# Performance work log

Measured on AMD Instinct MI355X. Metric: run time of the kernel, lower is better.

## Reference

```python
import jax, jax.numpy as jnp
import numpy as np

L, D, H, FF = 4, 256, 8, 4 * 256  # num_layers, d_model, nhead, ffn hidden
DK = D // H
EPS = 1e-5


def _ln(x, g, b):
    mu = jnp.mean(x, axis=-1, keepdims=True)
    var = jnp.mean(jnp.square(x - mu), axis=-1, keepdims=True)
    return (x - mu) * jax.lax.rsqrt(var + EPS) * g + b


def setup_inputs() -> dict:
    key = jax.random.key(0)
    ks = jax.random.split(key, 16)
    B, N = 8, 1024
    s = 0.02
    return {
        "x": jax.random.normal(ks[0], (B, N, D), jnp.float32),
        "coords": jax.random.normal(ks[1], (B, N, 3), jnp.float32),
        "Wq": jax.random.normal(ks[2], (L, D, D), jnp.float32) * s,
        "bq": jnp.zeros((L, D), jnp.float32),
        "Wk": jax.random.normal(ks[3], (L, D, D), jnp.float32) * s,
        "bk": jnp.zeros((L, D), jnp.float32),
        "Wv": jax.random.normal(ks[4], (L, D, D), jnp.float32) * s,
        "bv": jnp.zeros((L, D), jnp.float32),
        "alpha": jnp.full((L,), 0.1, jnp.float32),
        "W1": jax.random.normal(ks[5], (L, D, FF), jnp.float32) * s,
        "b1": jnp.zeros((L, FF), jnp.float32),
        "W2": jax.random.normal(ks[6], (L, FF, D), jnp.float32) * s,
        "b2": jnp.zeros((L, D), jnp.float32),
        "g1": jnp.ones((L, D), jnp.float32),
        "be1": jnp.zeros((L, D), jnp.float32),
        "g2": jnp.ones((L, D), jnp.float32),
        "be2": jnp.zeros((L, D), jnp.float32),
    }


def reference(x, coords, Wq, bq, Wk, bk, Wv, bv, alpha, W1, b1, W2, b2, g1, be1, g2, be2):
    B, N, _ = x.shape
    # Per-batch pairwise coord dot products (same math as the BN x BN matmul
    # sliced per batch in the original, computed without the cross-batch waste).
    G0 = jnp.einsum("bnc,bmc->bnm", coords, coords)  # [B,N,N]
    scale = 1.0 / jnp.sqrt(jnp.float32(DK))
    for i in range(L):
        q = (x @ Wq[i] + bq[i]).reshape(B, N, H, DK)
        k = (x @ Wk[i] + bk[i]).reshape(B, N, H, DK)
        v = (x @ Wv[i] + bv[i]).reshape(B, N, H, DK)
        scores = jnp.einsum("bnhd,bmhd->bhnm", q, k) * scale + (alpha[i] * G0)[:, None]
        attn = jax.nn.softmax(scores, axis=-1)
        out = jnp.einsum("bhnm,bmhd->bnhd", attn, v).reshape(B, N, D)
        x = _ln(x + out, g1[i], be1[i])
        ff = jnp.maximum(x @ W1[i] + b1[i], 0.0) @ W2[i] + b2[i]
        x = _ln(x + ff, g2[i], be2[i])
    return x
```

## Files before the change

kernel.cpp:

```cpp
#include <hip/hip_runtime.h>
#include <hip/hip_bf16.h>

#define BB 8
#define NN 1024
#define DD 256
#define HH 8
#define DK 32
#define FFN 1024
#define NLAYERS 4
#define MM (BB * NN)
#define ROW_ELEMS (MM * DD)

#define QSCALE 0.2550655192922103f
#define LOG2E  1.4426950408889634f

typedef unsigned short ushort_t;
typedef __attribute__((ext_vector_type(8))) short bf16x8;
typedef __attribute__((ext_vector_type(4))) short bf16x4;
typedef __attribute__((ext_vector_type(4))) float f32x4;

__device__ __forceinline__ f32x4 mfma16(bf16x4 a, bf16x4 b, f32x4 c) {
#if __has_builtin(__builtin_amdgcn_mfma_f32_16x16x16bf16_1k)
    return __builtin_amdgcn_mfma_f32_16x16x16bf16_1k(a, b, c, 0, 0, 0);
#elif defined(__AMDGCN__)
    f32x4 d;
    asm volatile("v_mfma_f32_16x16x16_bf16 %0, %1, %2, %3"
                 : "=v"(d)
                 : "v"(a), "v"(b), "v"(c));
    return d;
#else
    return c;
#endif
}

__device__ __forceinline__ ushort_t f2b(float f) {
    __hip_bfloat16 h = __float2bfloat16(f);
    return *reinterpret_cast<ushort_t*>(&h);
}

__device__ __forceinline__ float fast_exp2(float x) {
#if __has_builtin(__builtin_amdgcn_exp2f)
    return __builtin_amdgcn_exp2f(x);
#else
    return exp2f(x);
#endif
}

__device__ __forceinline__ void async_ld16(const void* g, void* l) {
    __builtin_amdgcn_global_load_lds((const __attribute__((address_space(1))) void*)g,
                                     (__attribute__((address_space(3))) void*)l, 16, 0, 0);
}

__global__ __launch_bounds__(256) void copy_in_kernel(const float* __restrict__ in,
                                                      float* __restrict__ xf,
                                                      ushort_t* __restrict__ xb, int n) {
    int i = blockIdx.x * 256 + threadIdx.x;
    if (i < n) { float v = in[i]; xf[i] = v; xb[i] = f2b(v); }
}

__global__ __launch_bounds__(256) void prep_kernel(const float* __restrict__ Wq,
                                                   const float* __restrict__ Wk,
                                                   const float* __restrict__ Wv,
                                                   const float* __restrict__ W1,
                                                   const float* __restrict__ W2,
                                                   const float* __restrict__ bq,
                                                   const float* __restrict__ bk,
                                                   const float* __restrict__ bv,
                                                   ushort_t* __restrict__ wqkvt,
                                                   ushort_t* __restrict__ w1t,
                                                   ushort_t* __restrict__ w2t,
                                                   float* __restrict__ bqkv) {
    const int id = blockIdx.x;
    const int layer = id / 707;
    const int r = id % 707;
    const int tid = threadIdx.x;

    if (r >= 704) {
        const int chunk = r - 704;
        const float* src = (chunk == 0) ? bq : (chunk == 1) ? bk : bv;
        bqkv[layer * 768 + chunk * 256 + tid] = src[layer * 256 + tid];
        return;
    }

    const float* src;
    ushort_t* dst;
    int R, C, x, y;
    if (r < 192) {
        const int w = r >> 6, rr = r & 63;
        src = ((w == 0) ? Wq : (w == 1) ? Wk : Wv) + (size_t)layer * 65536;
        dst = wqkvt + (size_t)layer * 196608 + w * 65536;
        R = 256; C = 256; x = rr & 7; y = rr >> 3;
    } else if (r < 448) {
        const int rr = r - 192;
        src = W1 + (size_t)layer * 262144;
        dst = w1t + (size_t)layer * 262144;
        R = 256; C = 1024; x = rr & 31; y = rr >> 5;
    } else {
        const int rr = r - 448;
        src = W2 + (size_t)layer * 262144;
        dst = w2t + (size_t)layer * 262144;
        R = 1024; C = 256; x = rr & 7; y = rr >> 3;
    }
    const int r0 = y * 32, c0 = x * 32;
    __shared__ float tile[32][33];
    const int tx = tid & 31, ty = tid >> 5;
#pragma unroll
    for (int i = 0; i < 4; ++i)
        tile[ty + 8 * i][tx] = src[(size_t)(r0 + ty + 8 * i) * C + (c0 + tx)];
    __syncthreads();
#pragma unroll
    for (int i = 0; i < 4; ++i)
        dst[(size_t)(c0 + ty + 8 * i) * R + (r0 + tx)] = f2b(tile[tx][ty + 8 * i]);
}

template <int MODE, int BM>
__global__ __launch_bounds__(256) void mfma_gemm_kernel(const ushort_t* __restrict__ A,
                                                        const ushort_t* __restrict__ Bt,
                                                        const float* __restrict__ bias,
                                                        void* __restrict__ C0,
                                                        void* __restrict__ C1,
                                                        void* __restrict__ C2,
                                                        const float* __restrict__ coords,
                                                        const float* __restrict__ alpha, int layer,
                                                        int K, int ldc) {
    constexpr int NI = BM / 32;
    __shared__ ushort_t As0[BM * 32];
    __shared__ ushort_t As1[BM * 32];
    __shared__ ushort_t Bs0[128 * 32];
    __shared__ ushort_t Bs1[128 * 32];

    const int t    = threadIdx.x;
    const int bm   = blockIdx.y * BM;
    const int bn   = blockIdx.x * 128;
    const int wave = t >> 6, lane = t & 63;
    const int wm   = (wave >> 1) * (BM / 2), wn = (wave & 1) * 64;
    const int quad = lane >> 4, l16 = lane & 15;

    const int srow = t >> 2;
    const int scol = (t & 3) * 8;

    f32x4 acc[NI][4];
#pragma unroll
    for (int i = 0; i < NI; ++i)
#pragma unroll
        for (int j = 0; j < 4; ++j) {
            f32x4 z = {0.f, 0.f, 0.f, 0.f};
            acc[i][j] = z;
        }

    for (int k0 = 0; k0 < K; k0 += 64) {
        __syncthreads();
        async_ld16(A + (size_t)(bm + srow) * K + k0 + scol, As0 + wave * 512);
        if constexpr (BM == 128)
            async_ld16(A + (size_t)(bm + 64 + srow) * K + k0 + scol, As0 + 2048 + wave * 512);
        async_ld16(Bt + (size_t)(bn + srow) * K + k0 + scol, Bs0 + wave * 512);
        async_ld16(Bt + (size_t)(bn + 64 + srow) * K + k0 + scol, Bs0 + 2048 + wave * 512);
        async_ld16(A + (size_t)(bm + srow) * K + k0 + 32 + scol, As1 + wave * 512);
        if constexpr (BM == 128)
            async_ld16(A + (size_t)(bm + 64 + srow) * K + k0 + 32 + scol, As1 + 2048 + wave * 512);
        async_ld16(Bt + (size_t)(bn + srow) * K + k0 + 32 + scol, Bs1 + wave * 512);
        async_ld16(Bt + (size_t)(bn + 64 + srow) * K + k0 + 32 + scol, Bs1 + 2048 + wave * 512);
        __syncthreads();

        bf16x8 af0[NI], af1[NI], bf0[4], bf1[4];
#pragma unroll
        for (int i = 0; i < NI; ++i) {
            af0[i] = *(const bf16x8*)(As0 + (wm + i * 16 + l16) * 32 + quad * 8);
            af1[i] = *(const bf16x8*)(As1 + (wm + i * 16 + l16) * 32 + quad * 8);
        }
#pragma unroll
        for (int j = 0; j < 4; ++j) {
            bf0[j] = *(const bf16x8*)(Bs0 + (wn + j * 16 + l16) * 32 + quad * 8);
            bf1[j] = *(const bf16x8*)(Bs1 + (wn + j * 16 + l16) * 32 + quad * 8);
        }
#pragma unroll
        for (int i = 0; i < NI; ++i)
#pragma unroll
            for (int j = 0; j < 4; ++j) {
                acc[i][j] = __builtin_amdgcn_mfma_f32_16x16x32_bf16(af0[i], bf0[j], acc[i][j], 0, 0, 0);
                acc[i][j] = __builtin_amdgcn_mfma_f32_16x16x32_bf16(af1[i], bf1[j], acc[i][j], 0, 0, 0);
            }
    }

    const float av = (MODE == 2) ? alpha[layer] : 0.f;

#pragma unroll
    for (int j = 0; j < 4; ++j) {
        const int col = bn + wn + j * 16 + l16;
        const float bsv = bias[col];
#pragma unroll
        for (int i = 0; i < NI; ++i) {
            const int row0 = bm + wm + i * 16 + quad * 4;
            if (MODE == 2) {
                const int bb2 = row0 >> 10, nn0 = row0 & 1023;
                const int which = col >> 8, rem = col & 255;
                const int h = rem >> 5, d = rem & 31;
                const size_t bh = (size_t)((bb2 << 3) + h);
                if (which == 2) {
                    ushort4 pk;
                    pk.x = f2b(acc[i][j][0] + bsv);
                    pk.y = f2b(acc[i][j][1] + bsv);
                    pk.z = f2b(acc[i][j][2] + bsv);
                    pk.w = f2b(acc[i][j][3] + bsv);
                    *(ushort4*)&((ushort_t*)C2)[(bh * DK + d) * NN + nn0] = pk;
                } else {
#pragma unroll
                    for (int r = 0; r < 4; ++r) {
                        const float v = acc[i][j][r] + bsv;
                        const int nn = nn0 + r;
                        if (which == 0) {
                            ((ushort_t*)C0)[(bh * NN + nn) * 64 + d] = f2b(v * QSCALE);
                            ushort_t ext = 0;
                            if (d < 3) ext = f2b(av * LOG2E * coords[(size_t)(bb2 * NN + nn) * 3 + d]);
                            ((ushort_t*)C0)[(bh * NN + nn) * 64 + 32 + d] = ext;
                        } else {
                            ((ushort_t*)C1)[(bh * NN + nn) * 64 + d] = f2b(v);
                            ushort_t ext = 0;
                            if (d < 3) ext = f2b(coords[(size_t)(bb2 * NN + nn) * 3 + d]);
                            ((ushort_t*)C1)[(bh * NN + nn) * 64 + 32 + d] = ext;
                        }
                    }
                }
            } else {
#pragma unroll
                for (int r = 0; r < 4; ++r) {
                    float v = acc[i][j][r] + bsv;
                    if (MODE == 0)
                        ((float*)C0)[(size_t)(row0 + r) * ldc + col] = v;
                    else
                        ((ushort_t*)C0)[(size_t)(row0 + r) * ldc + col] = f2b(fmaxf(v, 0.f));
                }
            }
        }
    }
}

__global__ __launch_bounds__(512) void ff2ln_kernel(const ushort_t* __restrict__ A,
                                                    const ushort_t* __restrict__ Bt,
                                                    const float* __restrict__ bias,
                                                    const float* __restrict__ xres,
                                                    const float* __restrict__ g,
                                                    const float* __restrict__ be,
                                                    float* __restrict__ xout,
                                                    ushort_t* __restrict__ xb) {
    constexpr int K = FFN;
    __shared__ ushort_t As0[32 * 32];
    __shared__ ushort_t As1[32 * 32];
    __shared__ ushort_t Bs0[256 * 32];
    __shared__ ushort_t Bs1[256 * 32];
    __shared__ float redS[8][32];
    __shared__ float redQ[8][32];

    const int t = threadIdx.x;
    const int bm = blockIdx.x * 32;
    const int wave = t >> 6, lane = t & 63;
    const int quad = lane >> 4, l16 = lane & 15;
    const int wn = wave * 32;
    const int srow = t >> 2;
    const int scol = (t & 3) * 8;

    f32x4 acc[2][2];
#pragma unroll
    for (int i = 0; i < 2; ++i)
#pragma unroll
        for (int j = 0; j < 2; ++j) {
            f32x4 z = {0.f, 0.f, 0.f, 0.f};
            acc[i][j] = z;
        }

    for (int k0 = 0; k0 < K; k0 += 64) {
        __syncthreads();
        if (t < 128) {
            async_ld16(A + (size_t)(bm + srow) * K + k0 + scol, As0 + wave * 512);
        } else if (t < 256) {
            async_ld16(A + (size_t)(bm + srow - 32) * K + k0 + 32 + scol, As1 + (wave - 2) * 512);
        }
        async_ld16(Bt + (size_t)srow * K + k0 + scol, Bs0 + wave * 512);
        async_ld16(Bt + (size_t)(128 + srow) * K + k0 + scol, Bs0 + 4096 + wave * 512);
        async_ld16(Bt + (size_t)srow * K + k0 + 32 + scol, Bs1 + wave * 512);
        async_ld16(Bt + (size_t)(128 + srow) * K + k0 + 32 + scol, Bs1 + 4096 + wave * 512);
        __syncthreads();

        bf16x8 af0[2], af1[2], bf0[2], bf1[2];
#pragma unroll
        for (int i = 0; i < 2; ++i) {
            af0[i] = *(const bf16x8*)(As0 + (i * 16 + l16) * 32 + quad * 8);
            af1[i] = *(const bf16x8*)(As1 + (i * 16 + l16) * 32 + quad * 8);
        }
#pragma unroll
        for (int j = 0; j < 2; ++j) {
            bf0[j] = *(const bf16x8*)(Bs0 + (wn + j * 16 + l16) * 32 + quad * 8);
            bf1[j] = *(const bf16x8*)(Bs1 + (wn + j * 16 + l16) * 32 + quad * 8);
        }
#pragma unroll
        for (int i = 0; i < 2; ++i)
#pragma unroll
            for (int j = 0; j < 2; ++j) {
                acc[i][j] = __builtin_amdgcn_mfma_f32_16x16x32_bf16(af0[i], bf0[j], acc[i][j], 0, 0, 0);
                acc[i][j] = __builtin_amdgcn_mfma_f32_16x16x32_bf16(af1[i], bf1[j], acc[i][j], 0, 0, 0);
            }
    }

    float mean[2][4], rstd[2][4];

    {
        float sum_[2][4];
#pragma unroll
        for (int i = 0; i < 2; ++i)
#pragma unroll
            for (int r = 0; r < 4; ++r) sum_[i][r] = 0.f;
#pragma unroll
        for (int j = 0; j < 2; ++j) {
            const int col = wn + j * 16 + l16;
            const float bj = bias[col];
#pragma unroll
            for (int i = 0; i < 2; ++i) {
                const int row = bm + i * 16 + quad * 4;
#pragma unroll
                for (int r = 0; r < 4; ++r) {
                    const float v = acc[i][j][r] + bj + xres[(size_t)(row + r) * DD + col];
                    acc[i][j][r] = v;
                    sum_[i][r] += v;
                }
            }
        }
#pragma unroll
        for (int i = 0; i < 2; ++i)
#pragma unroll
            for (int r = 0; r < 4; ++r) {
                float s = sum_[i][r];
                s += __shfl_xor(s, 1);
                s += __shfl_xor(s, 2);
                s += __shfl_xor(s, 4);
                s += __shfl_xor(s, 8);
                sum_[i][r] = s;
            }
        if (l16 == 0) {
#pragma unroll
            for (int i = 0; i < 2; ++i)
#pragma unroll
                for (int r = 0; r < 4; ++r) redS[wave][i * 16 + quad * 4 + r] = sum_[i][r];
        }
        __syncthreads();
#pragma unroll
        for (int i = 0; i < 2; ++i)
#pragma unroll
            for (int r = 0; r < 4; ++r) {
                const int rl = i * 16 + quad * 4 + r;
                float s = 0.f;
#pragma unroll
                for (int w = 0; w < 8; ++w) s += redS[w][rl];
                mean[i][r] = s * (1.0f / 256.0f);
            }
    }

    {
        float sq_[2][4];
#pragma unroll
        for (int i = 0; i < 2; ++i)
#pragma unroll
            for (int r = 0; r < 4; ++r) sq_[i][r] = 0.f;
#pragma unroll
        for (int j = 0; j < 2; ++j)
#pragma unroll
            for (int i = 0; i < 2; ++i)
#pragma unroll
                for (int r = 0; r < 4; ++r) {
                    const float d = acc[i][j][r] - mean[i][r];
                    sq_[i][r] += d * d;
                }
#pragma unroll
        for (int i = 0; i < 2; ++i)
#pragma unroll
            for (int r = 0; r < 4; ++r) {
                float s = sq_[i][r];
                s += __shfl_xor(s, 1);
                s += __shfl_xor(s, 2);
                s += __shfl_xor(s, 4);
                s += __shfl_xor(s, 8);
                sq_[i][r] = s;
            }
        if (l16 == 0) {
#pragma unroll
            for (int i = 0; i < 2; ++i)
#pragma unroll
                for (int r = 0; r < 4; ++r) redQ[wave][i * 16 + quad * 4 + r] = sq_[i][r];
        }
        __syncthreads();
#pragma unroll
        for (int i = 0; i < 2; ++i)
#pragma unroll
            for (int r = 0; r < 4; ++r) {
                const int rl = i * 16 + quad * 4 + r;
                float s = 0.f;
#pragma unroll
                for (int w = 0; w < 8; ++w) s += redQ[w][rl];
                rstd[i][r] = rsqrtf(s * (1.0f / 256.0f) + 1e-5f);
            }
    }

#pragma unroll
    for (int j = 0; j < 2; ++j) {
        const int col = wn + j * 16 + l16;
        const float gv = g[col];
        const float bev = be[col];
#pragma unroll
        for (int i = 0; i < 2; ++i) {
            const int row = bm + i * 16 + quad * 4;
#pragma unroll
            for (int r = 0; r < 4; ++r) {
                const float y = (acc[i][j][r] - mean[i][r]) * rstd[i][r] * gv + bev;
                xout[(size_t)(row + r) * DD + col] = y;
                xb[(size_t)(row + r) * DD + col] = f2b(y);
            }
        }
    }
}

__global__ __launch_bounds__(256, 2) void attn8_kernel(const ushort_t* __restrict__ Qa,
                                                       const ushort_t* __restrict__ Ka,
                                                       const ushort_t* __restrict__ Vt,
                                                       float* __restrict__ aout) {
    const int b = blockIdx.x, h = blockIdx.y, n0 = blockIdx.z * 64;
    const int t = threadIdx.x, wave = t >> 6, lane = t & 63;
    const int quad = lane >> 4, l16 = lane & 15;
    const int bh = b * HH + h;

    __shared__ __align__(16) char smem[56320];
    ushort_t (*Ks)[64][72] = (ushort_t (*)[64][72])smem;
    ushort_t (*Vs)[32][72] = (ushort_t (*)[32][72])(smem + 36864);
    float    (*Om)[64][36] = (float (*)[64][36])smem;
    float    (*Lm)[64]     = (float (*)[64])(smem + 55296);

    bf16x8 aq[4][2];
#pragma unroll
    for (int s = 0; s < 4; ++s) {
        const ushort_t* qp = Qa + ((size_t)bh * NN + n0 + s * 16 + l16) * 64 + quad * 8;
        aq[s][0] = *(const bf16x8*)qp;
        aq[s][1] = *(const bf16x8*)(qp + 32);
    }

    const f32x4 z = {0.f, 0.f, 0.f, 0.f};
    f32x4 acc[4][2];
    float lsum[4];
#pragma unroll
    for (int s = 0; s < 4; ++s) { acc[s][0] = z; acc[s][1] = z; lsum[s] = 0.f; }

    const ushort_t* kg = Ka + ((size_t)bh * NN + wave * 256) * 64;
    const ushort_t* vg = Vt + (size_t)bh * DK * NN + wave * 256;

    const int srow = lane >> 3, sch = (lane & 7) * 8;

    uint4 kreg[8], vreg[4];
#pragma unroll
    for (int i = 0; i < 8; ++i) kreg[i] = *(const uint4*)(kg + (size_t)(i * 8 + srow) * 64 + sch);
#pragma unroll
    for (int i = 0; i < 4; ++i) vreg[i] = *(const uint4*)(vg + (size_t)(i * 8 + srow) * NN + sch);

    for (int kt = 0; kt < 4; ++kt) {
#pragma unroll
        for (int i = 0; i < 8; ++i) *(uint4*)&Ks[wave][i * 8 + srow][sch] = kreg[i];
#pragma unroll
        for (int i = 0; i < 4; ++i) *(uint4*)&Vs[wave][i * 8 + srow][sch] = vreg[i];

        bf16x8 bk0[4], bk1[4];
#pragma unroll
        for (int jt = 0; jt < 4; ++jt) {
            bk0[jt] = *(const bf16x8*)&Ks[wave][jt * 16 + l16][quad * 8];
            bk1[jt] = *(const bf16x8*)&Ks[wave][jt * 16 + l16][32 + quad * 8];
        }
        bf16x4 vfrag[2][4];
#pragma unroll
        for (int g = 0; g < 2; ++g)
#pragma unroll
            for (int jt = 0; jt < 4; ++jt)
                vfrag[g][jt] = *(const bf16x4*)&Vs[wave][g * 16 + l16][jt * 16 + quad * 4];

        if (kt < 3) {
            const ushort_t* kg2 = kg + (size_t)(kt + 1) * 64 * 64;
            const ushort_t* vg2 = vg + (kt + 1) * 64;
#pragma unroll
            for (int i = 0; i < 8; ++i)
                kreg[i] = *(const uint4*)(kg2 + (size_t)(i * 8 + srow) * 64 + sch);
#pragma unroll
            for (int i = 0; i < 4; ++i)
                vreg[i] = *(const uint4*)(vg2 + (size_t)(i * 8 + srow) * NN + sch);
        }

#pragma unroll
        for (int s = 0; s < 4; ++s) {
            f32x4 st[4];
            __builtin_amdgcn_s_setprio(1);
#pragma unroll
            for (int jt = 0; jt < 4; ++jt) {
                st[jt] = __builtin_amdgcn_mfma_f32_16x16x32_bf16(bk0[jt], aq[s][0], z, 0, 0, 0);
                st[jt] = __builtin_amdgcn_mfma_f32_16x16x32_bf16(bk1[jt], aq[s][1], st[jt], 0, 0, 0);
            }
            __builtin_amdgcn_s_setprio(0);
            bf16x4 pf[4];
            float ls = 0.f;
#pragma unroll
            for (int jt = 0; jt < 4; ++jt) {
                float e0 = fast_exp2(st[jt][0]);
                float e1 = fast_exp2(st[jt][1]);
                float e2 = fast_exp2(st[jt][2]);
                float e3 = fast_exp2(st[jt][3]);
                ls += (e0 + e1) + (e2 + e3);
                pf[jt][0] = (short)f2b(e0);
                pf[jt][1] = (short)f2b(e1);
                pf[jt][2] = (short)f2b(e2);
                pf[jt][3] = (short)f2b(e3);
            }
            lsum[s] += ls;
            __builtin_amdgcn_s_setprio(1);
#pragma unroll
            for (int jt = 0; jt < 4; ++jt) {
                acc[s][0] = mfma16(vfrag[0][jt], pf[jt], acc[s][0]);
                acc[s][1] = mfma16(vfrag[1][jt], pf[jt], acc[s][1]);
            }
            __builtin_amdgcn_s_setprio(0);
        }
    }

#pragma unroll
    for (int s = 0; s < 4; ++s) {
        lsum[s] += __shfl_xor(lsum[s], 16);
        lsum[s] += __shfl_xor(lsum[s], 32);
    }

    __syncthreads();
    if (quad == 0) {
#pragma unroll
        for (int s = 0; s < 4; ++s) Lm[wave][s * 16 + l16] = lsum[s];
    }

#pragma unroll
    for (int s = 0; s < 4; ++s) {
        const int q = s * 16 + l16;
#pragma unroll
        for (int g = 0; g < 2; ++g) {
            float4 v = {acc[s][g][0], acc[s][g][1], acc[s][g][2], acc[s][g][3]};
            *(float4*)&Om[wave][q][g * 16 + quad * 4] = v;
        }
    }
    __syncthreads();

    {
        const int q = t >> 2, dseg = (t & 3) * 8;
        const float inv = 1.0f / (Lm[0][q] + Lm[1][q] + Lm[2][q] + Lm[3][q]);
        float* op = aout + (size_t)(b * NN + n0 + q) * DD + h * DK + dseg;
        float4 s0 = {0.f, 0.f, 0.f, 0.f}, s1 = {0.f, 0.f, 0.f, 0.f};
#pragma unroll
        for (int w = 0; w < 4; ++w) {
            float4 a = *(const float4*)&Om[w][q][dseg];
            float4 c = *(const float4*)&Om[w][q][dseg + 4];
            s0.x += a.x; s0.y += a.y; s0.z += a.z; s0.w += a.w;
            s1.x += c.x; s1.y += c.y; s1.z += c.z; s1.w += c.w;
        }
        float4 o0 = {s0.x * inv, s0.y * inv, s0.z * inv, s0.w * inv};
        float4 o1 = {s1.x * inv, s1.y * inv, s1.z * inv, s1.w * inv};
        *(float4*)op = o0;
        *(float4*)(op + 4) = o1;
    }
}

__global__ __launch_bounds__(256) void addln_kernel(const float* __restrict__ x,
                                                    ushort_t* __restrict__ xb,
                                                    const float* __restrict__ delta, int dstride,
                                                    const float* __restrict__ g,
                                                    const float* __restrict__ be,
                                                    float* __restrict__ xout) {
    const int row  = blockIdx.x * 4 + (threadIdx.x >> 6);
    const int lane = threadIdx.x & 63;
    const size_t base = (size_t)row * DD + lane * 4;

    float4 xv = *(const float4*)(x + base);
    float4 dl = *(const float4*)(delta + (size_t)row * dstride + lane * 4);
    float v0 = xv.x + dl.x, v1 = xv.y + dl.y, v2 = xv.z + dl.z, v3 = xv.w + dl.w;

    float s = v0 + v1 + v2 + v3;
#pragma unroll
    for (int off = 32; off; off >>= 1) s += __shfl_xor(s, off);
    const float mean = s * (1.0f / 256.0f);

    float d0 = v0 - mean, d1 = v1 - mean, d2 = v2 - mean, d3 = v3 - mean;
    float s2 = d0 * d0 + d1 * d1 + d2 * d2 + d3 * d3;
#pragma unroll
    for (int off = 32; off; off >>= 1) s2 += __shfl_xor(s2, off);
    const float rs = rsqrtf(s2 * (1.0f / 256.0f) + 1e-5f);

    float4 gv = *(const float4*)(g + lane * 4);
    float4 bv = *(const float4*)(be + lane * 4);
    float y0 = d0 * rs * gv.x + bv.x;
    float y1 = d1 * rs * gv.y + bv.y;
    float y2 = d2 * rs * gv.z + bv.z;
    float y3 = d3 * rs * gv.w + bv.w;

    float4 o = {y0, y1, y2, y3};
    *(float4*)(xout + base) = o;
    ushort4 ob = {f2b(y0), f2b(y1), f2b(y2), f2b(y3)};
    *(ushort4*)(xb + base) = ob;
}

extern "C" void kernel_launch(void* const* d_in, const int* in_sizes, int n_in,
                              void* d_out, int out_size, void* d_ws, size_t ws_size,
                              hipStream_t stream) {
    const float* x      = (const float*)d_in[0];
    const float* coords = (const float*)d_in[1];
    const float* Wq     = (const float*)d_in[2];
    const float* bq     = (const float*)d_in[3];
    const float* Wk     = (const float*)d_in[4];
    const float* bk     = (const float*)d_in[5];
    const float* Wv     = (const float*)d_in[6];
    const float* bv     = (const float*)d_in[7];
    const float* alpha  = (const float*)d_in[8];
    const float* W1     = (const float*)d_in[9];
    const float* b1     = (const float*)d_in[10];
    const float* W2     = (const float*)d_in[11];
    const float* b2     = (const float*)d_in[12];
    const float* g1     = (const float*)d_in[13];
    const float* be1    = (const float*)d_in[14];
    const float* g2     = (const float*)d_in[15];
    const float* be2    = (const float*)d_in[16];

    float* ws = (float*)d_ws;
    float*    xf    = ws;
    ushort_t* xb    = (ushort_t*)(ws + 2097152);
    ushort_t* Qa    = (ushort_t*)(ws + 3145728);
    ushort_t* Ka    = (ushort_t*)(ws + 5242880);
    ushort_t* Vt    = (ushort_t*)(ws + 7340032);
    float*    aout  = ws + 8388608;
    ushort_t* wqkvt = (ushort_t*)(ws + 10485760);
    ushort_t* w1t   = (ushort_t*)(ws + 10878976);
    ushort_t* w2t   = (ushort_t*)(ws + 11403264);
    float*    bqkv  = ws + 11927552;

    ushort_t* hidden = Qa;

    prep_kernel<<<NLAYERS * 707, 256, 0, stream>>>(Wq, Wk, Wv, W1, W2, bq, bk, bv,
                                                   wqkvt, w1t, w2t, bqkv);

    copy_in_kernel<<<ROW_ELEMS / 256, 256, 0, stream>>>(x, xf, xb, ROW_ELEMS);

    for (int i = 0; i < NLAYERS; ++i) {
        mfma_gemm_kernel<2, 64><<<dim3(6, 128), 256, 0, stream>>>(
            xb, wqkvt + (size_t)i * 196608, bqkv + i * 768, Qa, Ka, Vt,
            coords, alpha, i, 256, 0);

        attn8_kernel<<<dim3(8, 8, 16), 256, 0, stream>>>(Qa, Ka, Vt, aout);

        addln_kernel<<<MM / 4, 256, 0, stream>>>(xf, xb, aout, 256, g1 + i * 256, be1 + i * 256, xf);

        mfma_gemm_kernel<1, 128><<<dim3(8, 64), 256, 0, stream>>>(
            xb, w1t + (size_t)i * 262144, b1 + i * 1024, hidden, nullptr, nullptr,
            nullptr, nullptr, 0, 256, 1024);

        ff2ln_kernel<<<MM / 32, 512, 0, stream>>>(
            hidden, w2t + (size_t)i * 262144, b2 + i * 256, xf,
            g2 + i * 256, be2 + i * 256,
            (i == NLAYERS - 1) ? (float*)d_out : xf, xb);
    }
}
```

Before: 413.0 us.

## Load GEMM fragments directly from global into registers with double buffering

Replaces the LDS-staged GEMM mainloops (global_load_lds plus barriers) in the QKV/FFN1 GEMM and the fused FF2+LN kernel with direct per-lane global loads into MFMA fragment registers, ping-ponging two register buffers to overlap the next tile's loads with the current MFMAs. The FFN1 GEMM now uses 64-row tiles (doubling its grid), and the input copy kernel is vectorised to float4. This removes LDS traffic and block barriers, but each wave now fetches its own operands from global/L2 with no sharing inside the block, which raises redundant memory traffic and register pressure.

```diff
diff --git a/kernel.cpp b/kernel.cpp
--- a/kernel.cpp
+++ b/kernel.cpp
@@ -46,16 +46,16 @@
 #endif
 }
 
-__device__ __forceinline__ void async_ld16(const void* g, void* l) {
-    __builtin_amdgcn_global_load_lds((const __attribute__((address_space(1))) void*)g,
-                                     (__attribute__((address_space(3))) void*)l, 16, 0, 0);
-}
-
-__global__ __launch_bounds__(256) void copy_in_kernel(const float* __restrict__ in,
-                                                      float* __restrict__ xf,
-                                                      ushort_t* __restrict__ xb, int n) {
+__global__ __launch_bounds__(256) void copy_in_kernel(const float4* __restrict__ in,
+                                                      float4* __restrict__ xf,
+                                                      ushort4* __restrict__ xb, int n4) {
     int i = blockIdx.x * 256 + threadIdx.x;
-    if (i < n) { float v = in[i]; xf[i] = v; xb[i] = f2b(v); }
+    if (i < n4) {
+        float4 v = in[i];
+        xf[i] = v;
+        ushort4 b = {f2b(v.x), f2b(v.y), f2b(v.z), f2b(v.w)};
+        xb[i] = b;
+    }
 }
 
 __global__ __launch_bounds__(256) void prep_kernel(const float* __restrict__ Wq,
@@ -113,31 +113,27 @@
         dst[(size_t)(c0 + ty + 8 * i) * R + (r0 + tx)] = f2b(tile[tx][ty + 8 * i]);
 }
 
-template <int MODE, int BM>
-__global__ __launch_bounds__(256) void mfma_gemm_kernel(const ushort_t* __restrict__ A,
-                                                        const ushort_t* __restrict__ Bt,
-                                                        const float* __restrict__ bias,
-                                                        void* __restrict__ C0,
-                                                        void* __restrict__ C1,
-                                                        void* __restrict__ C2,
-                                                        const float* __restrict__ coords,
-                                                        const float* __restrict__ alpha, int layer,
-                                                        int K, int ldc) {
-    constexpr int NI = BM / 32;
-    __shared__ ushort_t As0[BM * 32];
-    __shared__ ushort_t As1[BM * 32];
-    __shared__ ushort_t Bs0[128 * 32];
-    __shared__ ushort_t Bs1[128 * 32];
-
+template <int MODE>
+__global__ __launch_bounds__(256) void rgemm_kernel(const ushort_t* __restrict__ A,
+                                                    const ushort_t* __restrict__ Bt,
+                                                    const float* __restrict__ bias,
+                                                    void* __restrict__ C0,
+                                                    void* __restrict__ C1,
+                                                    void* __restrict__ C2,
+                                                    const float* __restrict__ coords,
+                                                    const float* __restrict__ alpha, int layer,
+                                                    int K, int ldc) {
+    constexpr int NI = 2;
     const int t    = threadIdx.x;
-    const int bm   = blockIdx.y * BM;
+    const int bm   = blockIdx.y * 64;
     const int bn   = blockIdx.x * 128;
     const int wave = t >> 6, lane = t & 63;
-    const int wm   = (wave >> 1) * (BM / 2), wn = (wave & 1) * 64;
+    const int wm   = (wave >> 1) * 32, wn = (wave & 1) * 64;
     const int quad = lane >> 4, l16 = lane & 15;
 
-    const int srow = t >> 2;
-    const int scol = (t & 3) * 8;
+    const ushort_t* ap = A + (size_t)(bm + wm + l16) * K + quad * 8;
+    const ushort_t* bp = Bt + (size_t)(bn + wn + l16) * K + quad * 8;
+    const size_t K16 = (size_t)16 * K;
 
     f32x4 acc[NI][4];
 #pragma unroll
@@ -148,39 +144,36 @@
             acc[i][j] = z;
         }
 
-    for (int k0 = 0; k0 < K; k0 += 64) {
-        __syncthreads();
-        async_ld16(A + (size_t)(bm + srow) * K + k0 + scol, As0 + wave * 512);
-        if constexpr (BM == 128)
-            async_ld16(A + (size_t)(bm + 64 + srow) * K + k0 + scol, As0 + 2048 + wave * 512);
-        async_ld16(Bt + (size_t)(bn + srow) * K + k0 + scol, Bs0 + wave * 512);
-        async_ld16(Bt + (size_t)(bn + 64 + srow) * K + k0 + scol, Bs0 + 2048 + wave * 512);
-        async_ld16(A + (size_t)(bm + srow) * K + k0 + 32 + scol, As1 + wave * 512);
-        if constexpr (BM == 128)
-            async_ld16(A + (size_t)(bm + 64 + srow) * K + k0 + 32 + scol, As1 + 2048 + wave * 512);
-        async_ld16(Bt + (size_t)(bn + srow) * K + k0 + 32 + scol, Bs1 + wave * 512);
-        async_ld16(Bt + (size_t)(bn + 64 + srow) * K + k0 + 32 + scol, Bs1 + 2048 + wave * 512);
-        __syncthreads();
-
-        bf16x8 af0[NI], af1[NI], bf0[4], bf1[4];
-#pragma unroll
-        for (int i = 0; i < NI; ++i) {
-            af0[i] = *(const bf16x8*)(As0 + (wm + i * 16 + l16) * 32 + quad * 8);
-            af1[i] = *(const bf16x8*)(As1 + (wm + i * 16 + l16) * 32 + quad * 8);
-        }
-#pragma unroll
-        for (int j = 0; j < 4; ++j) {
-            bf0[j] = *(const bf16x8*)(Bs0 + (wn + j * 16 + l16) * 32 + quad * 8);
-            bf1[j] = *(const bf16x8*)(Bs1 + (wn + j * 16 + l16) * 32 + quad * 8);
-        }
-#pragma unroll
-        for (int i = 0; i < NI; ++i)
-#pragma unroll
-            for (int j = 0; j < 4; ++j) {
-                acc[i][j] = __builtin_amdgcn_mfma_f32_16x16x32_bf16(af0[i], bf0[j], acc[i][j], 0, 0, 0);
-                acc[i][j] = __builtin_amdgcn_mfma_f32_16x16x32_bf16(af1[i], bf1[j], acc[i][j], 0, 0, 0);
-            }
-    }
+    bf16x8 aA[2][2], bA[2][4], aB[2][2], bB[2][4];
+
+#define G_LOAD_TILE(aa, bb, k0)                                          \
+    {                                                                    \
+        _Pragma("unroll") for (int i = 0; i < 2; ++i) {                  \
+            aa[0][i] = *(const bf16x8*)(ap + i * K16 + (k0));            \
+            aa[1][i] = *(const bf16x8*)(ap + i * K16 + (k0) + 32);       \
+        }                                                                \
+        _Pragma("unroll") for (int j = 0; j < 4; ++j) {                  \
+            bb[0][j] = *(const bf16x8*)(bp + j * K16 + (k0));            \
+            bb[1][j] = *(const bf16x8*)(bp + j * K16 + (k0) + 32);       \
+        }                                                                \
+    }
+
+#define G_MFMA_TILE(aa, bb)                                              \
+    _Pragma("unroll") for (int i = 0; i < 2; ++i)                        \
+    _Pragma("unroll") for (int j = 0; j < 4; ++j) {                      \
+        acc[i][j] = __builtin_amdgcn_mfma_f32_16x16x32_bf16(aa[0][i], bb[0][j], acc[i][j], 0, 0, 0); \
+        acc[i][j] = __builtin_amdgcn_mfma_f32_16x16x32_bf16(aa[1][i], bb[1][j], acc[i][j], 0, 0, 0); \
+    }
+
+    G_LOAD_TILE(aA, bA, 0)
+    for (int k0 = 0; k0 < K; k0 += 128) {
+        G_LOAD_TILE(aB, bB, k0 + 64)
+        G_MFMA_TILE(aA, bA)
+        if (k0 + 128 < K) G_LOAD_TILE(aA, bA, k0 + 128)
+        G_MFMA_TILE(aB, bB)
+    }
+#undef G_LOAD_TILE
+#undef G_MFMA_TILE
 
     const float av = (MODE == 2) ? alpha[layer] : 0.f;
 
@@ -244,10 +237,6 @@
                                                     float* __restrict__ xout,
                                                     ushort_t* __restrict__ xb) {
     constexpr int K = FFN;
-    __shared__ ushort_t As0[32 * 32];
-    __shared__ ushort_t As1[32 * 32];
-    __shared__ ushort_t Bs0[256 * 32];
-    __shared__ ushort_t Bs1[256 * 32];
     __shared__ float redS[8][32];
     __shared__ float redQ[8][32];
 
@@ -256,8 +245,10 @@
     const int wave = t >> 6, lane = t & 63;
     const int quad = lane >> 4, l16 = lane & 15;
     const int wn = wave * 32;
-    const int srow = t >> 2;
-    const int scol = (t & 3) * 8;
+
+    const ushort_t* ap = A + (size_t)(bm + l16) * K + quad * 8;
+    const ushort_t* bp = Bt + (size_t)(wn + l16) * K + quad * 8;
+    const size_t K16 = (size_t)16 * K;
 
     f32x4 acc[2][2];
 #pragma unroll
@@ -268,38 +259,36 @@
             acc[i][j] = z;
         }
 
-    for (int k0 = 0; k0 < K; k0 += 64) {
-        __syncthreads();
-        if (t < 128) {
-            async_ld16(A + (size_t)(bm + srow) * K + k0 + scol, As0 + wave * 512);
-        } else if (t < 256) {
-            async_ld16(A + (size_t)(bm + srow - 32) * K + k0 + 32 + scol, As1 + (wave - 2) * 512);
-        }
-        async_ld16(Bt + (size_t)srow * K + k0 + scol, Bs0 + wave * 512);
-        async_ld16(Bt + (size_t)(128 + srow) * K + k0 + scol, Bs0 + 4096 + wave * 512);
-        async_ld16(Bt + (size_t)srow * K + k0 + 32 + scol, Bs1 + wave * 512);
-        async_ld16(Bt + (size_t)(128 + srow) * K + k0 + 32 + scol, Bs1 + 4096 + wave * 512);
-        __syncthreads();
-
-        bf16x8 af0[2], af1[2], bf0[2], bf1[2];
-#pragma unroll
-        for (int i = 0; i < 2; ++i) {
-            af0[i] = *(const bf16x8*)(As0 + (i * 16 + l16) * 32 + quad * 8);
-            af1[i] = *(const bf16x8*)(As1 + (i * 16 + l16) * 32 + quad * 8);
-        }
-#pragma unroll
-        for (int j = 0; j < 2; ++j) {
-            bf0[j] = *(const bf16x8*)(Bs0 + (wn + j * 16 + l16) * 32 + quad * 8);
-            bf1[j] = *(const bf16x8*)(Bs1 + (wn + j * 16 + l16) * 32 + quad * 8);
-        }
-#pragma unroll
-        for (int i = 0; i < 2; ++i)
-#pragma unroll
-            for (int j = 0; j < 2; ++j) {
-                acc[i][j] = __builtin_amdgcn_mfma_f32_16x16x32_bf16(af0[i], bf0[j], acc[i][j], 0, 0, 0);
-                acc[i][j] = __builtin_amdgcn_mfma_f32_16x16x32_bf16(af1[i], bf1[j], acc[i][j], 0, 0, 0);
-            }
-    }
+    bf16x8 aA[2][2], bA[2][2], aB[2][2], bB[2][2];
+
+#define F_LOAD_TILE(aa, bb, k0)                                          \
+    {                                                                    \
+        _Pragma("unroll") for (int i = 0; i < 2; ++i) {                  \
+            aa[0][i] = *(const bf16x8*)(ap + i * K16 + (k0));            \
+            aa[1][i] = *(const bf16x8*)(ap + i * K16 + (k0) + 32);       \
+        }                                                                \
+        _Pragma("unroll") for (int j = 0; j < 2; ++j) {                  \
+            bb[0][j] = *(const bf16x8*)(bp + j * K16 + (k0));            \
+            bb[1][j] = *(const bf16x8*)(bp + j * K16 + (k0) + 32);       \
+        }                                                                \
+    }
+
+#define F_MFMA_TILE(aa, bb)                                              \
+    _Pragma("unroll") for (int i = 0; i < 2; ++i)                        \
+    _Pragma("unroll") for (int j = 0; j < 2; ++j) {                      \
+        acc[i][j] = __builtin_amdgcn_mfma_f32_16x16x32_bf16(aa[0][i], bb[0][j], acc[i][j], 0, 0, 0); \
+        acc[i][j] = __builtin_amdgcn_mfma_f32_16x16x32_bf16(aa[1][i], bb[1][j], acc[i][j], 0, 0, 0); \
+    }
+
+    F_LOAD_TILE(aA, bA, 0)
+    for (int k0 = 0; k0 < K; k0 += 128) {
+        F_LOAD_TILE(aB, bB, k0 + 64)
+        F_MFMA_TILE(aA, bA)
+        if (k0 + 128 < K) F_LOAD_TILE(aA, bA, k0 + 128)
+        F_MFMA_TILE(aB, bB)
+    }
+#undef F_LOAD_TILE
+#undef F_MFMA_TILE
 
     float mean[2][4], rstd[2][4];
 
@@ -640,10 +629,11 @@
     prep_kernel<<<NLAYERS * 707, 256, 0, stream>>>(Wq, Wk, Wv, W1, W2, bq, bk, bv,
                                                    wqkvt, w1t, w2t, bqkv);
 
-    copy_in_kernel<<<ROW_ELEMS / 256, 256, 0, stream>>>(x, xf, xb, ROW_ELEMS);
+    copy_in_kernel<<<ROW_ELEMS / 4 / 256, 256, 0, stream>>>((const float4*)x, (float4*)xf,
+                                                            (ushort4*)xb, ROW_ELEMS / 4);
 
     for (int i = 0; i < NLAYERS; ++i) {
-        mfma_gemm_kernel<2, 64><<<dim3(6, 128), 256, 0, stream>>>(
+        rgemm_kernel<2><<<dim3(6, 128), 256, 0, stream>>>(
             xb, wqkvt + (size_t)i * 196608, bqkv + i * 768, Qa, Ka, Vt,
             coords, alpha, i, 256, 0);
 
@@ -651,7 +641,7 @@
 
         addln_kernel<<<MM / 4, 256, 0, stream>>>(xf, xb, aout, 256, g1 + i * 256, be1 + i * 256, xf);
 
-        mfma_gemm_kernel<1, 128><<<dim3(8, 64), 256, 0, stream>>>(
+        rgemm_kernel<1><<<dim3(8, 128), 256, 0, stream>>>(
             xb, w1t + (size_t)i * 262144, b1 + i * 1024, hidden, nullptr, nullptr,
             nullptr, nullptr, 0, 256, 1024);
 
```

Result: slower. 554.2 us (+34.2%).

## Double-buffer LDS tiles in GEMM kernels and vectorize input copy

Applied to the files above, without the earlier changes.

The MFMA GEMM and FF2+LayerNorm kernels now double-buffer their shared-memory tiles. The next K-slice's async global-to-LDS loads are issued before computing on the current slice, so each iteration needs one barrier instead of two. This aims to hide global load latency behind MFMA work, at the cost of doubling LDS use per block, which can reduce occupancy. The input copy kernel also moves to float4 loads and stores to cut the instruction count.

```diff
diff --git a/kernel.cpp b/kernel.cpp
--- a/kernel.cpp
+++ b/kernel.cpp
@@ -51,11 +51,16 @@
                                      (__attribute__((address_space(3))) void*)l, 16, 0, 0);
 }
 
-__global__ __launch_bounds__(256) void copy_in_kernel(const float* __restrict__ in,
-                                                      float* __restrict__ xf,
-                                                      ushort_t* __restrict__ xb, int n) {
+__global__ __launch_bounds__(256) void copy_in_kernel(const float4* __restrict__ in,
+                                                      float4* __restrict__ xf,
+                                                      ushort4* __restrict__ xb, int n4) {
     int i = blockIdx.x * 256 + threadIdx.x;
-    if (i < n) { float v = in[i]; xf[i] = v; xb[i] = f2b(v); }
+    if (i < n4) {
+        float4 v = in[i];
+        xf[i] = v;
+        ushort4 b = {f2b(v.x), f2b(v.y), f2b(v.z), f2b(v.w)};
+        xb[i] = b;
+    }
 }
 
 __global__ __launch_bounds__(256) void prep_kernel(const float* __restrict__ Wq,
@@ -124,10 +129,10 @@
                                                         const float* __restrict__ alpha, int layer,
                                                         int K, int ldc) {
     constexpr int NI = BM / 32;
-    __shared__ ushort_t As0[BM * 32];
-    __shared__ ushort_t As1[BM * 32];
-    __shared__ ushort_t Bs0[128 * 32];
-    __shared__ ushort_t Bs1[128 * 32];
+    __shared__ ushort_t As0[2][BM * 32];
+    __shared__ ushort_t As1[2][BM * 32];
+    __shared__ ushort_t Bs0[2][128 * 32];
+    __shared__ ushort_t Bs1[2][128 * 32];
 
     const int t    = threadIdx.x;
     const int bm   = blockIdx.y * BM;
@@ -148,30 +153,36 @@
             acc[i][j] = z;
         }
 
-    for (int k0 = 0; k0 < K; k0 += 64) {
+    auto stage = [&](int pb, int k0) {
+        async_ld16(A + (size_t)(bm + srow) * K + k0 + scol, As0[pb] + wave * 512);
+        if constexpr (BM == 128)
+            async_ld16(A + (size_t)(bm + 64 + srow) * K + k0 + scol, As0[pb] + 2048 + wave * 512);
+        async_ld16(Bt + (size_t)(bn + srow) * K + k0 + scol, Bs0[pb] + wave * 512);
+        async_ld16(Bt + (size_t)(bn + 64 + srow) * K + k0 + scol, Bs0[pb] + 2048 + wave * 512);
+        async_ld16(A + (size_t)(bm + srow) * K + k0 + 32 + scol, As1[pb] + wave * 512);
+        if constexpr (BM == 128)
+            async_ld16(A + (size_t)(bm + 64 + srow) * K + k0 + 32 + scol, As1[pb] + 2048 + wave * 512);
+        async_ld16(Bt + (size_t)(bn + srow) * K + k0 + 32 + scol, Bs1[pb] + wave * 512);
+        async_ld16(Bt + (size_t)(bn + 64 + srow) * K + k0 + 32 + scol, Bs1[pb] + 2048 + wave * 512);
+    };
+
+    stage(0, 0);
+    int pb = 0;
+    for (int k0 = 0; k0 < K; k0 += 64, pb ^= 1) {
         __syncthreads();
-        async_ld16(A + (size_t)(bm + srow) * K + k0 + scol, As0 + wave * 512);
-        if constexpr (BM == 128)
-            async_ld16(A + (size_t)(bm + 64 + srow) * K + k0 + scol, As0 + 2048 + wave * 512);
-        async_ld16(Bt + (size_t)(bn + srow) * K + k0 + scol, Bs0 + wave * 512);
-        async_ld16(Bt + (size_t)(bn + 64 + srow) * K + k0 + scol, Bs0 + 2048 + wave * 512);
-        async_ld16(A + (size_t)(bm + srow) * K + k0 + 32 + scol, As1 + wave * 512);
-        if constexpr (BM == 128)
-            async_ld16(A + (size_t)(bm + 64 + srow) * K + k0 + 32 + scol, As1 + 2048 + wave * 512);
-        async_ld16(Bt + (size_t)(bn + srow) * K + k0 + 32 + scol, Bs1 + wave * 512);
-        async_ld16(Bt + (size_t)(bn + 64 + srow) * K + k0 + 32 + scol, Bs1 + 2048 + wave * 512);
-        __syncthreads();
+
+        if (k0 + 64 < K) stage(pb ^ 1, k0 + 64);
 
         bf16x8 af0[NI], af1[NI], bf0[4], bf1[4];
 #pragma unroll
         for (int i = 0; i < NI; ++i) {
-            af0[i] = *(const bf16x8*)(As0 + (wm + i * 16 + l16) * 32 + quad * 8);
-            af1[i] = *(const bf16x8*)(As1 + (wm + i * 16 + l16) * 32 + quad * 8);
+            af0[i] = *(const bf16x8*)(As0[pb] + (wm + i * 16 + l16) * 32 + quad * 8);
+            af1[i] = *(const bf16x8*)(As1[pb] + (wm + i * 16 + l16) * 32 + quad * 8);
         }
 #pragma unroll
         for (int j = 0; j < 4; ++j) {
-            bf0[j] = *(const bf16x8*)(Bs0 + (wn + j * 16 + l16) * 32 + quad * 8);
-            bf1[j] = *(const bf16x8*)(Bs1 + (wn + j * 16 + l16) * 32 + quad * 8);
+            bf0[j] = *(const bf16x8*)(Bs0[pb] + (wn + j * 16 + l16) * 32 + quad * 8);
+            bf1[j] = *(const bf16x8*)(Bs1[pb] + (wn + j * 16 + l16) * 32 + quad * 8);
         }
 #pragma unroll
         for (int i = 0; i < NI; ++i)
@@ -244,10 +255,10 @@
                                                     float* __restrict__ xout,
                                                     ushort_t* __restrict__ xb) {
     constexpr int K = FFN;
-    __shared__ ushort_t As0[32 * 32];
-    __shared__ ushort_t As1[32 * 32];
-    __shared__ ushort_t Bs0[256 * 32];
-    __shared__ ushort_t Bs1[256 * 32];
+    __shared__ ushort_t As0[2][32 * 32];
+    __shared__ ushort_t As1[2][32 * 32];
+    __shared__ ushort_t Bs0[2][256 * 32];
+    __shared__ ushort_t Bs1[2][256 * 32];
     __shared__ float redS[8][32];
     __shared__ float redQ[8][32];
 
@@ -268,29 +279,35 @@
             acc[i][j] = z;
         }
 
-    for (int k0 = 0; k0 < K; k0 += 64) {
+    auto stage = [&](int pb, int k0) {
+        if (t < 128) {
+            async_ld16(A + (size_t)(bm + srow) * K + k0 + scol, As0[pb] + wave * 512);
+        } else if (t < 256) {
+            async_ld16(A + (size_t)(bm + srow - 32) * K + k0 + 32 + scol, As1[pb] + (wave - 2) * 512);
+        }
+        async_ld16(Bt + (size_t)srow * K + k0 + scol, Bs0[pb] + wave * 512);
+        async_ld16(Bt + (size_t)(128 + srow) * K + k0 + scol, Bs0[pb] + 4096 + wave * 512);
+        async_ld16(Bt + (size_t)srow * K + k0 + 32 + scol, Bs1[pb] + wave * 512);
+        async_ld16(Bt + (size_t)(128 + srow) * K + k0 + 32 + scol, Bs1[pb] + 4096 + wave * 512);
+    };
+
+    stage(0, 0);
+    int pb = 0;
+    for (int k0 = 0; k0 < K; k0 += 64, pb ^= 1) {
         __syncthreads();
-        if (t < 128) {
-            async_ld16(A + (size_t)(bm + srow) * K + k0 + scol, As0 + wave * 512);
-        } else if (t < 256) {
-            async_ld16(A + (size_t)(bm + srow - 32) * K + k0 + 32 + scol, As1 + (wave - 2) * 512);
-        }
-        async_ld16(Bt + (size_t)srow * K + k0 + scol, Bs0 + wave * 512);
-        async_ld16(Bt + (size_t)(128 + srow) * K + k0 + scol, Bs0 + 4096 + wave * 512);
-        async_ld16(Bt + (size_t)srow * K + k0 + 32 + scol, Bs1 + wave * 512);
-        async_ld16(Bt + (size_t)(128 + srow) * K + k0 + 32 + scol, Bs1 + 4096 + wave * 512);
-        __syncthreads();
+
+        if (k0 + 64 < K) stage(pb ^ 1, k0 + 64);
 
         bf16x8 af0[2], af1[2], bf0[2], bf1[2];
 #pragma unroll
         for (int i = 0; i < 2; ++i) {
-            af0[i] = *(const bf16x8*)(As0 + (i * 16 + l16) * 32 + quad * 8);
-            af1[i] = *(const bf16x8*)(As1 + (i * 16 + l16) * 32 + quad * 8);
+            af0[i] = *(const bf16x8*)(As0[pb] + (i * 16 + l16) * 32 + quad * 8);
+            af1[i] = *(const bf16x8*)(As1[pb] + (i * 16 + l16) * 32 + quad * 8);
         }
 #pragma unroll
         for (int j = 0; j < 2; ++j) {
-            bf0[j] = *(const bf16x8*)(Bs0 + (wn + j * 16 + l16) * 32 + quad * 8);
-            bf1[j] = *(const bf16x8*)(Bs1 + (wn + j * 16 + l16) * 32 + quad * 8);
+            bf0[j] = *(const bf16x8*)(Bs0[pb] + (wn + j * 16 + l16) * 32 + quad * 8);
+            bf1[j] = *(const bf16x8*)(Bs1[pb] + (wn + j * 16 + l16) * 32 + quad * 8);
         }
 #pragma unroll
         for (int i = 0; i < 2; ++i)
@@ -640,7 +657,8 @@
     prep_kernel<<<NLAYERS * 707, 256, 0, stream>>>(Wq, Wk, Wv, W1, W2, bq, bk, bv,
                                                    wqkvt, w1t, w2t, bqkv);
 
-    copy_in_kernel<<<ROW_ELEMS / 256, 256, 0, stream>>>(x, xf, xb, ROW_ELEMS);
+    copy_in_kernel<<<ROW_ELEMS / 4 / 256, 256, 0, stream>>>((const float4*)x, (float4*)xf,
+                                                            (ushort4*)xb, ROW_ELEMS / 4);
 
     for (int i = 0; i < NLAYERS; ++i) {
         mfma_gemm_kernel<2, 64><<<dim3(6, 128), 256, 0, stream>>>(
```

Measured after the change: 410.3 us. About the same (-0.6%).
